# Kernel tuning notes

Hardware: AMD Instinct MI355X
Metric: run time of the kernel (lower is better)

The kernel has to match this reference:

```python
import jax, jax.numpy as jnp
import numpy as np

B, T, C = 4, 4096, 1024


def setup_inputs() -> dict:
    key = jax.random.key(0)
    k_x, k_f, k_g, k_p = jax.random.split(key, 4)
    scale = 1.0 / np.sqrt(C)  # keep gate pre-activations well-scaled
    return {
        "x": jax.random.normal(k_x, (B, T, C), dtype=jnp.float32),
        "W_f_x": jax.random.normal(k_f, (C, C), dtype=jnp.float32) * scale,
        "W_g_x": jax.random.normal(k_g, (C, C), dtype=jnp.float32) * scale,
        "W_proj": jax.random.normal(k_p, (C, C), dtype=jnp.float32) * scale,
    }


def _cfc_scan(a, b):
    """Solve h_t = a_t * h_{t-1} + b_t with h_{-1}=0 along axis 1 (T).

    Associative op on linear maps: (A_l,B_l) then (A_r,B_r) composes to
    (A_r*A_l, A_r*B_l + B_r). With h_init=0, h_t = B-component.
    """
    def op(l, r):
        al, bl = l
        ar, br = r
        return ar * al, ar * bl + br
    _, h = jax.lax.associative_scan(op, (a, b), axis=1)
    return h


def reference(x, W_f_x, W_g_x, W_proj):
    # Gates depend on x only (parallel mode). nn.Linear: x @ W.T
    f = jax.nn.sigmoid(jnp.einsum("btc,dc->btd", x, W_f_x))  # (B,T,C)
    g = jnp.tanh(jnp.einsum("btc,dc->btd", x, W_g_x))        # (B,T,C)
    h = _cfc_scan(f, (1.0 - f) * g)                           # (B,T,C)
    return jnp.einsum("btc,dc->btd", h, W_proj)               # c_proj
```

## Files before the change

kernel.cpp:

```cpp
#include <hip/hip_runtime.h>
#include <hip/hip_bf16.h>
#include <stdint.h>

#define TT 4096
#define BB 4
#define CC 1024
#define MM (BB * TT)
#define NCHUNK 64
#define CHUNK_T (TT / NCHUNK)
#define NCHAIN (BB * CC)

typedef float f32x4 __attribute__((ext_vector_type(4)));
typedef __bf16 bf16x8 __attribute__((ext_vector_type(8)));
typedef ushort us8 __attribute__((ext_vector_type(8)));

__device__ __forceinline__ float b2f(ushort u) {
  union { float f; uint32_t v; } x; x.v = ((uint32_t)u) << 16; return x.f;
}
__device__ __forceinline__ ushort f2b(float f) {
  union { float f; uint32_t u; } x; x.f = f;
  uint32_t r = x.u + 0x7fffu + ((x.u >> 16) & 1u);
  return (ushort)(r >> 16);
}

__device__ __forceinline__ void async_copy16(const ushort* g, ushort* l) {
  __builtin_amdgcn_global_load_lds(
      (__attribute__((address_space(1))) void*)(g),
      (__attribute__((address_space(3))) void*)(l), 16, 0, 0);
}

__global__ __launch_bounds__(256) void cvt_all(const float* __restrict__ x,
                                               const float* __restrict__ wf,
                                               const float* __restrict__ wg,
                                               const float* __restrict__ wp,
                                               ushort* __restrict__ xb,
                                               ushort* __restrict__ wcat,
                                               ushort* __restrict__ wpb) {
  const int i = blockIdx.x * 256 + threadIdx.x;
  const float* s; ushort* d; int off, dst;
  if (i < 4194304) {
    s = x; d = xb; off = i; dst = i;
  } else if (i < 4456448) {
    s = wf; d = wcat; off = i - 4194304;
    dst = ((off >> 8) << 9) + (off & 255);
  } else if (i < 4718592) {
    s = wg; d = wcat; off = i - 4456448;
    dst = ((off >> 8) << 9) + 256 + (off & 255);
  } else {
    s = wp; d = wpb; off = i - 4718592; dst = off;
  }
  float4 v = ((const float4*)s)[off];
  ushort4 o;
  o.x = f2b(v.x); o.y = f2b(v.y); o.z = f2b(v.z); o.w = f2b(v.w);
  ((ushort4*)d)[dst] = o;
}


#define RDA(sl, ih)                                                       \
  _Pragma("unroll") for (int i_ = 0; i_ < 4; ++i_)                        \
      af[i_] = *(const bf16x8*)(rA + (sl) * 8192 + (ih) * 2048 + i_ * 512);

#define RDB(sl)                                                           \
  _Pragma("unroll") for (int j_ = 0; j_ < 4; ++j_)                        \
      bfr[j_] = *(const bf16x8*)(rB + (sl) * 8192 + j_ * 512);

#define MFMA16(ih)                                                        \
  __builtin_amdgcn_s_setprio(1);                                          \
  _Pragma("unroll") for (int i_ = 0; i_ < 4; ++i_)                        \
  _Pragma("unroll") for (int j_ = 0; j_ < 4; ++j_)                        \
      acc[(ih) * 4 + i_][j_] = __builtin_amdgcn_mfma_f32_16x16x32_bf16(   \
          bfr[j_], af[i_], acc[(ih) * 4 + i_][j_], 0, 0, 0);              \
  __builtin_amdgcn_s_setprio(0)

#define MIDBAR()                                                          \
  __builtin_amdgcn_s_barrier();                                           \
  asm volatile("s_waitcnt lgkmcnt(0)" ::: "memory");                      \
  __builtin_amdgcn_sched_barrier(0)

#define ENDBAR()                                                          \
  __builtin_amdgcn_s_barrier();                                           \
  __builtin_amdgcn_sched_barrier(0)

#define CK4() asm volatile("s_waitcnt vmcnt(4)" ::: "memory")
#define CK0() asm volatile("s_waitcnt vmcnt(0)" ::: "memory")

#define TILE(S0, S1, NS0, NS1, KN)                                        \
  RDA(S0, 0); RDB(S0); stageA(NS0, (KN));      MIDBAR(); MFMA16(0);        ENDBAR(); \
  RDA(S0, 1);          stageB(NS0, (KN));      MIDBAR(); MFMA16(1); CK4(); ENDBAR(); \
  RDA(S1, 0); RDB(S1); stageA(NS1, (KN) + 32); MIDBAR(); MFMA16(0);        ENDBAR(); \
  RDA(S1, 1);          stageB(NS1, (KN) + 32); MIDBAR(); MFMA16(1); CK4(); ENDBAR();

#define BFLY16(Av, Bv)                                                    \
  _Pragma("unroll") for (int m_ = 1; m_ < 16; m_ <<= 1) {                 \
    float Ao_ = __shfl_xor(Av, m_);                                       \
    float Bo_ = __shfl_xor(Bv, m_);                                       \
    Bv = ((lane & m_) == 0) ? fmaf(Ao_, Bv, Bo_) : fmaf(Av, Bo_, Bv);     \
    Av = Ao_ * Av;                                                        \
  }

template <int MODE>
__global__ __launch_bounds__(512, 2) void gemm_bt(const ushort* __restrict__ A,
                                                  const ushort* __restrict__ Bw,
                                                  float* __restrict__ outF,
                                                  ushort* __restrict__ outB,
                                                  float* __restrict__ cA2,
                                                  float* __restrict__ cB2, int N) {
  constexpr int K = CC;
  __shared__ __align__(16) ushort sA[4 * 256 * 32];
  __shared__ __align__(16) ushort sB[4 * 256 * 32];

  const int tid = threadIdx.x;
  const int lane = tid & 63;
  const int w = tid >> 6;
  const int wm = w >> 2;
  const int wn = w & 3;

  const int nbx = N >> 8;
  const int cpx = (int)gridDim.x >> 3;
  const int bid = blockIdx.x;
  const int wg = (bid & 7) * cpx + (bid >> 3);
  const long n0 = (long)(wg % nbx) << 8;
  const long m0 = (long)(wg / nbx) << 8;

  const int srow = lane >> 2;
  const int goct = (lane & 3) ^ ((lane >> 3) & 3);
  const ushort* gA0 = A + (m0 + w * 16 + srow) * K + goct * 8;
  const ushort* gB0 = Bw + (n0 + w * 16 + srow) * K + goct * 8;
  const ushort* gA1 = gA0 + 128 * (long)K;
  const ushort* gB1 = gB0 + 128 * (long)K;
  ushort* dA0 = &sA[w * 512 + lane * 8];
  ushort* dA1 = dA0 + 4096;
  ushort* dB0 = &sB[w * 512 + lane * 8];
  ushort* dB1 = dB0 + 4096;

  auto stageA = [&](int slot, int koff) {
    async_copy16(gA0 + koff, dA0 + slot * 8192);
    async_copy16(gA1 + koff, dA1 + slot * 8192);
  };
  auto stageB = [&](int slot, int koff) {
    async_copy16(gB0 + koff, dB0 + slot * 8192);
    async_copy16(gB1 + koff, dB1 + slot * 8192);
  };

  const int rlo = lane & 15;
  const int kq = lane >> 4;
  const int oslot = kq ^ ((rlo >> 1) & 3);
  const ushort* rA = &sA[(wm * 128 + rlo) * 32 + oslot * 8];
  const ushort* rB = &sB[(wn * 64 + rlo) * 32 + oslot * 8];

  f32x4 acc[8][4];
#pragma unroll
  for (int i = 0; i < 8; ++i)
#pragma unroll
    for (int j = 0; j < 4; ++j) acc[i][j] = (f32x4){0.f, 0.f, 0.f, 0.f};

  bf16x8 af[4], bfr[4];

  stageA(0, 0);
  stageB(0, 0);
  stageA(1, 32);
  stageB(1, 32);
  CK4();
  ENDBAR();

  for (int t2 = 0; t2 < 7; ++t2) {
    const int kn = t2 * 128 + 64;
    TILE(0, 1, 2, 3, kn);
    TILE(2, 3, 0, 1, kn + 64);
  }
  TILE(0, 1, 2, 3, 960);
  RDA(2, 0); RDB(2); MIDBAR(); MFMA16(0); ENDBAR();
  RDA(2, 1);         MIDBAR(); MFMA16(1); CK0(); ENDBAR();
  RDA(3, 0); RDB(3); MIDBAR(); MFMA16(0); ENDBAR();
  RDA(3, 1);         MIDBAR(); MFMA16(1);

  const int mloc = lane & 15;
  const int nq = (lane >> 4) * 4;

  if (MODE == 0) {
#pragma unroll
    for (int i = 0; i < 8; ++i) {
      const long m = m0 + wm * 128 + i * 16 + mloc;
#pragma unroll
      for (int j = 0; j < 4; ++j) {
        const long nb = n0 + wn * 64 + j * 16 + nq;
        *(f32x4*)(outF + m * N + nb) = acc[i][j];
      }
    }
  } else {
    const int kq4 = lane >> 4;
    const long bIdx = m0 >> 12;
    const int t0 = (int)(m0 & 4095) + wm * 128;
    const long chb = (n0 >> 1) + wn * 32;
#pragma unroll
    for (int cp = 0; cp < 2; ++cp) {
      float CA[4][2], CB[4][2];
#pragma unroll
      for (int hh = 0; hh < 4; ++hh) {
        const int i = cp * 4 + hh;
        const long m = m0 + wm * 128 + i * 16 + mloc;
#pragma unroll
        for (int j = 0; j < 4; ++j) {
          const long nb = n0 + wn * 64 + j * 16 + nq;
          const f32x4 v = acc[i][j];
          float act0 = __builtin_amdgcn_rcpf(1.f + __expf(-v[0]));
          float act1 = fmaf(-2.f, __builtin_amdgcn_rcpf(1.f + __expf(2.f * v[1])), 1.f);
          float act2 = __builtin_amdgcn_rcpf(1.f + __expf(-v[2]));
          float act3 = fmaf(-2.f, __builtin_amdgcn_rcpf(1.f + __expf(2.f * v[3])), 1.f);
          ushort4 o;
          o.x = f2b(act0); o.y = f2b(act1); o.z = f2b(act2); o.w = f2b(act3);
          *(ushort4*)(outB + m * (long)N + nb) = o;
          const float fr0 = b2f(o.x), gr0 = b2f(o.y);
          const float fr1 = b2f(o.z), gr1 = b2f(o.w);
          float a0 = fr0, b0 = (1.f - fr0) * gr0;
          float a1 = fr1, b1 = (1.f - fr1) * gr1;
          BFLY16(a0, b0);
          BFLY16(a1, b1);
          if (hh == 0) {
            CA[j][0] = a0; CB[j][0] = b0;
            CA[j][1] = a1; CB[j][1] = b1;
          } else {
            CB[j][0] = fmaf(a0, CB[j][0], b0); CA[j][0] *= a0;
            CB[j][1] = fmaf(a1, CB[j][1], b1); CA[j][1] *= a1;
          }
        }
      }
      if (mloc == 0) {
        const int gchunk = (t0 >> 6) + cp;
#pragma unroll
        for (int j = 0; j < 4; ++j) {
          const long ch0 = chb + j * 8 + kq4 * 2;
          const long i0 = (bIdx * CC + ch0) * 64 + gchunk;
          cA2[i0] = CA[j][0];       cB2[i0] = CB[j][0];
          cA2[i0 + 64] = CA[j][1];  cB2[i0 + 64] = CB[j][1];
        }
      }
    }
  }
}

__global__ __launch_bounds__(256) void scan_pass2(const float* __restrict__ cA2,
                                                  const float* __restrict__ cB2,
                                                  float* __restrict__ h2) {
  const int gid = blockIdx.x * 256 + threadIdx.x;
  const int chain = gid >> 6;
  const int lane = threadIdx.x & 63;
  float Av = cA2[chain * 64 + lane];
  float Bv = cB2[chain * 64 + lane];
#pragma unroll
  for (int m = 1; m < 64; m <<= 1) {
    const float Ao = __shfl_up(Av, m);
    const float Bo = __shfl_up(Bv, m);
    if (lane >= m) { Bv = fmaf(Av, Bo, Bv); Av = Av * Ao; }
  }
  const float Bx = __shfl_up(Bv, 1);
  h2[chain * 64 + lane] = (lane == 0) ? 0.f : Bx;
}

__global__ __launch_bounds__(256) void scan_pass3(const ushort* __restrict__ P,
                                                  const float* __restrict__ h2,
                                                  ushort* __restrict__ H) {
  const int pc = blockIdx.x * 256 + threadIdx.x;
  const int chunk = blockIdx.y;
  const int b = pc >> 8, c4 = (pc & 255) * 4;
  float h[4];
#pragma unroll
  for (int r = 0; r < 4; ++r) h[r] = h2[(b * CC + c4 + r) * 64 + chunk];
  const us8* p =
      (const us8*)(P + (size_t)(b * TT + chunk * CHUNK_T) * (2 * CC) + c4 * 2);
  ushort4* hp = (ushort4*)(H + (size_t)(b * TT + chunk * CHUNK_T) * CC + c4);
#pragma unroll 4
  for (int i = 0; i < CHUNK_T; ++i) {
    const us8 v = p[0];
    p += 2 * CC / 8;
    ushort4 o;
#pragma unroll
    for (int r = 0; r < 4; ++r) {
      const float f = b2f(v[2 * r]);
      const float g = b2f(v[2 * r + 1]);
      h[r] = fmaf(f, h[r], (1.f - f) * g);
    }
    o.x = f2b(h[0]); o.y = f2b(h[1]); o.z = f2b(h[2]); o.w = f2b(h[3]);
    *hp = o;
    hp += CC / 4;
  }
}

extern "C" void kernel_launch(void* const* d_in, const int* in_sizes, int n_in,
                              void* d_out, int out_size, void* d_ws, size_t ws_size,
                              hipStream_t stream) {
  const float* x  = (const float*)d_in[0];
  const float* Wf = (const float*)d_in[1];
  const float* Wg = (const float*)d_in[2];
  const float* Wp = (const float*)d_in[3];

  char* ws = (char*)d_ws;
  ushort* xb   = (ushort*)(ws);
  ushort* Hb   = xb;
  ushort* Wcat = (ushort*)(ws + 33554432);
  ushort* Wpb  = (ushort*)(ws + 33554432 + 4194304);
  ushort* P    = (ushort*)(ws + 33554432 + 4194304 + 2097152);
  char* tail   = ws + 33554432 + 4194304 + 2097152 + 67108864;
  float* cA2   = (float*)(tail);
  float* cB2   = (float*)(tail + 1048576);
  float* h2    = (float*)(tail + 2097152);
  (void)ws_size; (void)in_sizes; (void)n_in; (void)out_size;

  cvt_all<<<19456, 256, 0, stream>>>(x, Wf, Wg, Wp, xb, Wcat, Wpb);

  gemm_bt<1><<<512, 512, 0, stream>>>(xb, Wcat, nullptr, P, cA2, cB2, 2 * CC);

  scan_pass2<<<NCHAIN * 64 / 256, 256, 0, stream>>>(cA2, cB2, h2);
  dim3 gs(NCHAIN / 4 / 256, NCHUNK);
  scan_pass3<<<gs, 256, 0, stream>>>(P, h2, Hb);

  gemm_bt<0><<<256, 512, 0, stream>>>(Hb, Wpb, (float*)d_out, nullptr, nullptr, nullptr, CC);
}
```

Baseline: 269.9 us.

## Replace shuffle butterfly chunk scan with LDS transpose and serial per-lane scan

```diff
diff --git a/kernel.cpp b/kernel.cpp
--- a/kernel.cpp
+++ b/kernel.cpp
@@ -90,14 +90,6 @@
   RDA(S1, 0); RDB(S1); stageA(NS1, (KN) + 32); MIDBAR(); MFMA16(0);        ENDBAR(); \
   RDA(S1, 1);          stageB(NS1, (KN) + 32); MIDBAR(); MFMA16(1); CK4(); ENDBAR();
 
-#define BFLY16(Av, Bv)                                                    \
-  _Pragma("unroll") for (int m_ = 1; m_ < 16; m_ <<= 1) {                 \
-    float Ao_ = __shfl_xor(Av, m_);                                       \
-    float Bo_ = __shfl_xor(Bv, m_);                                       \
-    Bv = ((lane & m_) == 0) ? fmaf(Ao_, Bv, Bo_) : fmaf(Av, Bo_, Bv);     \
-    Av = Ao_ * Av;                                                        \
-  }
-
 template <int MODE>
 __global__ __launch_bounds__(512, 2) void gemm_bt(const ushort* __restrict__ A,
                                                   const ushort* __restrict__ Bw,
@@ -188,52 +180,65 @@
       }
     }
   } else {
-    const int kq4 = lane >> 4;
     const long bIdx = m0 >> 12;
     const int t0 = (int)(m0 & 4095) + wm * 128;
     const long chb = (n0 >> 1) + wn * 32;
-#pragma unroll
-    for (int cp = 0; cp < 2; ++cp) {
-      float CA[4][2], CB[4][2];
-#pragma unroll
-      for (int hh = 0; hh < 4; ++hh) {
-        const int i = cp * 4 + hh;
+    float* slab = (float*)((w < 4) ? &sA[w * 8192] : &sB[(w - 4) * 8192]);
+    __builtin_amdgcn_s_barrier();
+    __builtin_amdgcn_sched_barrier(0);
+
+    const int chl = lane & 31;
+    const int thf = lane >> 5;
+#pragma unroll
+    for (int rd = 0; rd < 2; ++rd) {
+#pragma unroll
+      for (int ii = 0; ii < 4; ++ii) {
+        const int i = rd * 4 + ii;
         const long m = m0 + wm * 128 + i * 16 + mloc;
+        const int tl = ii * 16 + mloc;
 #pragma unroll
         for (int j = 0; j < 4; ++j) {
           const long nb = n0 + wn * 64 + j * 16 + nq;
           const f32x4 v = acc[i][j];
-          float act0 = __builtin_amdgcn_rcpf(1.f + __expf(-v[0]));
-          float act1 = fmaf(-2.f, __builtin_amdgcn_rcpf(1.f + __expf(2.f * v[1])), 1.f);
-          float act2 = __builtin_amdgcn_rcpf(1.f + __expf(-v[2]));
-          float act3 = fmaf(-2.f, __builtin_amdgcn_rcpf(1.f + __expf(2.f * v[3])), 1.f);
+          float f0 = __builtin_amdgcn_rcpf(1.f + __expf(-v[0]));
+          float g0 = fmaf(-2.f, __builtin_amdgcn_rcpf(1.f + __expf(2.f * v[1])), 1.f);
+          float f1 = __builtin_amdgcn_rcpf(1.f + __expf(-v[2]));
+          float g1 = fmaf(-2.f, __builtin_amdgcn_rcpf(1.f + __expf(2.f * v[3])), 1.f);
           ushort4 o;
-          o.x = f2b(act0); o.y = f2b(act1); o.z = f2b(act2); o.w = f2b(act3);
+          o.x = f2b(f0); o.y = f2b(g0); o.z = f2b(f1); o.w = f2b(g1);
           *(ushort4*)(outB + m * (long)N + nb) = o;
           const float fr0 = b2f(o.x), gr0 = b2f(o.y);
           const float fr1 = b2f(o.z), gr1 = b2f(o.w);
-          float a0 = fr0, b0 = (1.f - fr0) * gr0;
-          float a1 = fr1, b1 = (1.f - fr1) * gr1;
-          BFLY16(a0, b0);
-          BFLY16(a1, b1);
-          if (hh == 0) {
-            CA[j][0] = a0; CB[j][0] = b0;
-            CA[j][1] = a1; CB[j][1] = b1;
-          } else {
-            CB[j][0] = fmaf(a0, CB[j][0], b0); CA[j][0] *= a0;
-            CB[j][1] = fmaf(a1, CB[j][1], b1); CA[j][1] *= a1;
-          }
+          const int c0 = j * 8 + (nq >> 1);
+          float2 p0; p0.x = fr0; p0.y = (1.f - fr0) * gr0;
+          float2 p1; p1.x = fr1; p1.y = (1.f - fr1) * gr1;
+          *(float2*)(slab + (c0 * 64 + (tl ^ c0)) * 2) = p0;
+          *(float2*)(slab + ((c0 + 1) * 64 + (tl ^ (c0 + 1))) * 2) = p1;
         }
       }
-      if (mloc == 0) {
-        const int gchunk = (t0 >> 6) + cp;
-#pragma unroll
-        for (int j = 0; j < 4; ++j) {
-          const long ch0 = chb + j * 8 + kq4 * 2;
-          const long i0 = (bIdx * CC + ch0) * 64 + gchunk;
-          cA2[i0] = CA[j][0];       cB2[i0] = CB[j][0];
-          cA2[i0 + 64] = CA[j][1];  cB2[i0 + 64] = CB[j][1];
-        }
+      asm volatile("s_waitcnt lgkmcnt(0)" ::: "memory");
+      __builtin_amdgcn_sched_barrier(0);
+      float Av = 1.f, Bv = 0.f;
+#pragma unroll
+      for (int s = 0; s < 32; ++s) {
+        const int t = thf * 32 + s;
+        const float2 ab = *(const float2*)(slab + (chl * 64 + (t ^ chl)) * 2);
+        Bv = fmaf(ab.x, Bv, ab.y);
+        Av *= ab.x;
+      }
+      const float Ao = __shfl_xor(Av, 32);
+      const float Bo = __shfl_xor(Bv, 32);
+      const float Af = (thf == 0) ? Ao * Av : Av * Ao;
+      const float Bf = (thf == 0) ? fmaf(Ao, Bv, Bo) : fmaf(Av, Bo, Bv);
+      if (thf == 0) {
+        const int gchunk = (t0 >> 6) + rd;
+        const long i0 = (bIdx * CC + chb + chl) * 64 + gchunk;
+        cA2[i0] = Af;
+        cB2[i0] = Bf;
+      }
+      if (rd == 0) {
+        asm volatile("s_waitcnt lgkmcnt(0)" ::: "memory");
+        __builtin_amdgcn_sched_barrier(0);
       }
     }
   }
```

Measured after the change: 256.0 us. 1.05x faster.
